# Kernel optimization log

Measured on AMD Instinct MI355X. Metric: run time of the kernel, lower is better.

The kernel has to match this reference:

```python
import jax, jax.numpy as jnp
import numpy as np

B, S, D = 8, 512, 256          # batch, seq_len, input_depth
E, H = 8, 4                    # num_experts, num_heads
DK = DV = DO = 256             # total_key/value/output depth (per expert)
DH = DK // H                   # head dim = 64
SCALE = DH ** -0.5


def setup_inputs() -> dict:
    key = jax.random.key(0)
    ks = jax.random.split(key, 8)
    queries = jax.random.normal(ks[0], (B, S, D), jnp.float32)
    keys = jax.random.normal(ks[1], (B, S, D), jnp.float32)
    values = jax.random.normal(ks[2], (B, S, D), jnp.float32)
    mask = jax.random.randint(ks[3], (B, S, S), 0, 2).astype(bool)
    s = 0.05
    Wq = jax.random.normal(ks[4], (D, DK * E), jnp.float32) * s
    Wk = jax.random.normal(ks[5], (D, DK * E), jnp.float32) * s
    Wv = jax.random.normal(ks[6], (D, DV * E), jnp.float32) * s
    Wo = jax.random.normal(ks[7], (DV, DO * E), jnp.float32) * s
    return {"queries": queries, "keys": keys, "values": values, "mask": mask,
            "Wq": Wq, "Wk": Wk, "Wv": Wv, "Wo": Wo}


def _split_heads(x):
    # [B, S, E*H*DH] -> [B, E, H, S, DH]
    b, s, _ = x.shape
    return x.reshape(b, s, E, H, -1).transpose(0, 2, 3, 1, 4)


def reference(queries, keys, values, mask, Wq, Wk, Wv, Wo):
    q = _split_heads(queries @ Wq) * SCALE   # [B,E,H,S,DH]
    k = _split_heads(keys @ Wk)
    v = _split_heads(values @ Wv)
    logits = jnp.einsum('behqd,behkd->behqk', q, k)      # [B,E,H,S,S]
    m = mask[:, None, None].astype(jnp.float32)          # [B,1,1,S,S]
    logits = logits * (1.0 - m) + (-1e18) * m
    w = jax.nn.softmax(logits, axis=-1)
    ctx = jnp.einsum('behqk,behkd->behqd', w, v)         # [B,E,H,S,DH]
    # merge heads -> [B, S, E, H*DH]
    ctx = ctx.transpose(0, 3, 1, 2, 4).reshape(B, S, E, H * DH)
    # faithful quirk: Dense applied on rank-4 tensor -> [B,S,E,DO*E]
    return ctx @ Wo
```

## Files before the change

kernel.cpp:

```cpp
#include <hip/hip_runtime.h>
#include <stdint.h>


typedef __bf16 bf16x8 __attribute__((ext_vector_type(8)));
typedef float f32x4 __attribute__((ext_vector_type(4)));
typedef unsigned short u16x8 __attribute__((ext_vector_type(8)));
typedef unsigned short u16x4 __attribute__((ext_vector_type(4)));

#define MFMA16(a, b, c) __builtin_amdgcn_mfma_f32_16x16x32_bf16(a, b, c, 0, 0, 0)

__device__ __forceinline__ unsigned short bfc(float x) {
    __bf16 b = (__bf16)x;
    return __builtin_bit_cast(unsigned short, b);
}

__device__ __forceinline__ void gload16(const void* g, void* l) {
    __builtin_amdgcn_global_load_lds(
        (const __attribute__((address_space(1))) void*)g,
        (__attribute__((address_space(3))) void*)l, 16, 0, 0);
}

#define QSCALE 0.18033688011112042f
#define MASKVAL -28.853900817779268f

__global__ __launch_bounds__(256) void prep_kern(
        const float* __restrict__ q, const float* __restrict__ k,
        const float* __restrict__ v, const int* __restrict__ mask,
        const float* __restrict__ Wq, const float* __restrict__ Wk,
        const float* __restrict__ Wv, const float* __restrict__ Wo,
        unsigned short* __restrict__ qb, unsigned short* __restrict__ kb,
        unsigned short* __restrict__ vb, unsigned short* __restrict__ wt,
        uint32_t* __restrict__ maskbits) {
    __shared__ float tile[32][33];
    const int x = blockIdx.x, t = threadIdx.x;
    if (x < 3072) {
        int which = x >> 10;
        const float* s = (which == 0) ? q : (which == 1) ? k : v;
        unsigned short* o = (which == 0) ? qb : (which == 1) ? kb : vb;
        int i = ((x & 1023) * 256 + t) * 4;
        float4 f = *(const float4*)&s[i];
        u16x4 r;
        r[0] = bfc(f.x); r[1] = bfc(f.y); r[2] = bfc(f.z); r[3] = bfc(f.w);
        *(u16x4*)&o[i] = r;
    } else if (x < 5120) {
        int y = x - 3072;
        int wsel = y >> 9;
        const float* W = (wsel == 0) ? Wq : (wsel == 1) ? Wk : (wsel == 2) ? Wv : Wo;
        unsigned short* T = wt + wsel * 2048 * 256;
        int rem = y & 511;
        int c0 = (rem & 63) * 32, r0 = (rem >> 6) * 32;
        int tr = t >> 3, tc = (t & 7) * 4;
        float4 f = *(const float4*)&W[(r0 + tr) * 2048 + c0 + tc];
        tile[tr][tc + 0] = f.x; tile[tr][tc + 1] = f.y;
        tile[tr][tc + 2] = f.z; tile[tr][tc + 3] = f.w;
        __syncthreads();
        u16x4 o;
        o[0] = bfc(tile[tc + 0][tr]); o[1] = bfc(tile[tc + 1][tr]);
        o[2] = bfc(tile[tc + 2][tr]); o[3] = bfc(tile[tc + 3][tr]);
        *(u16x4*)&T[(c0 + tr) * 256 + r0 + tc] = o;
    } else {
        const int lane = t & 63;
        int wi = ((x - 5120) * 4 + (t >> 6)) * 32;
        for (int i = 0; i < 32; ++i) {
            int u = wi + i;
            int b = u >> 12, rem = u & 4095, row = rem >> 3, ktp = rem & 7;
            int mv = mask[((size_t)(b * 512 + row)) * 512 + ktp * 64 + lane];
            unsigned long long bal = __ballot(mv != 0);
            if (lane == 0) {
                maskbits[(size_t)(b * 16 + ktp * 2) * 512 + row] = (uint32_t)bal;
                maskbits[(size_t)(b * 16 + ktp * 2 + 1) * 512 + row] = (uint32_t)(bal >> 32);
            }
        }
    }
}

__global__ __launch_bounds__(1024) void fused_kern(
        const unsigned short* __restrict__ actq,
        const unsigned short* __restrict__ actk,
        const unsigned short* __restrict__ actv,
        const unsigned short* __restrict__ Wt,
        const uint32_t* __restrict__ maskbits,
        unsigned short* __restrict__ CTX) {
    __shared__ unsigned short Klds[512 * 64];
    __shared__ unsigned short Vt[64 * 512];
    __shared__ unsigned short R3[2][64 * 128];
    const int bid = (int)blockIdx.x;
    const int flat = (bid & 7) * 32 + (bid >> 3);
    const int b = flat >> 5, eh = flat & 31;
    const int e = eh >> 2, h = eh & 3;
    const int t = threadIdx.x, w = t >> 6, l = t & 63, li = l & 15, g = l >> 4;
    const int tw0 = w * 32;
    const size_t actoff = (size_t)b * 512 * 256;
    const size_t wso = ((size_t)(e * 256 + h * 64)) * 256;

    bf16x8 qf[2][2];

    auto STAGEW = [&](int unit) {
        const unsigned short* W = Wt + (size_t)(unit >> 1) * 2048 * 256 + wso +
                                  (unit & 1) * 128;
        const int nr = (w << 2) + (l >> 4), cic = l & 15;
        gload16(&W[(size_t)nr * 256 + ((cic ^ (nr & 7)) << 3)],
                &R3[unit & 1][w * 512]);
    };

    STAGEW(0);
    __syncthreads();

    for (int p = 0; p < 3; ++p) {
        const unsigned short* A = ((p == 0) ? actq : (p == 1) ? actk : actv) + actoff;
        f32x4 acc[2][4];
#pragma unroll
        for (int m = 0; m < 2; ++m)
#pragma unroll
            for (int n = 0; n < 4; ++n) acc[m][n] = (f32x4){0.f, 0.f, 0.f, 0.f};
#pragma unroll
        for (int kh = 0; kh < 2; ++kh) {
            const int unit = p * 2 + kh;
            if (unit < 5) STAGEW(unit + 1);
            const unsigned short* cur = R3[unit & 1];
#pragma unroll
            for (int kk = 0; kk < 4; ++kk) {
                const int k0 = kh * 128 + kk * 32;
                bf16x8 af[2], bfr[4];
#pragma unroll
                for (int m = 0; m < 2; ++m)
                    af[m] = *(const bf16x8*)&A[(size_t)(tw0 + m * 16 + li) * 256 + k0 + g * 8];
#pragma unroll
                for (int n = 0; n < 4; ++n) {
                    int nr = n * 16 + li;
                    bfr[n] = *(const bf16x8*)&cur[nr * 128 + ((kk * 32 + g * 8) ^ ((nr & 7) << 3))];
                }
                if (p == 2) {
#pragma unroll
                    for (int m = 0; m < 2; ++m)
#pragma unroll
                        for (int n = 0; n < 4; ++n)
                            acc[m][n] = MFMA16(af[m], bfr[n], acc[m][n]);
                } else {
#pragma unroll
                    for (int m = 0; m < 2; ++m)
#pragma unroll
                        for (int n = 0; n < 4; ++n)
                            acc[m][n] = MFMA16(bfr[n], af[m], acc[m][n]);
                }
            }
            __syncthreads();
        }
        if (p == 0) {
            unsigned short* qs = Klds + w * 2048;
#pragma unroll
            for (int m = 0; m < 2; ++m)
#pragma unroll
                for (int n = 0; n < 4; ++n) {
                    int row = m * 16 + li, dh = n * 16 + g * 4;
                    u16x4 o;
#pragma unroll
                    for (int i = 0; i < 4; ++i) o[i] = bfc(acc[m][n][i] * QSCALE);
                    *(u16x4*)&qs[row * 64 + (dh ^ ((row & 7) << 3))] = o;
                }
#pragma unroll
            for (int m = 0; m < 2; ++m) {
                int row = m * 16 + li;
                qf[m][0] = *(const bf16x8*)&qs[row * 64 + ((g * 8) ^ ((row & 7) << 3))];
                qf[m][1] = *(const bf16x8*)&qs[row * 64 + ((32 + g * 8) ^ ((row & 7) << 3))];
            }
        } else if (p == 1) {
#pragma unroll
            for (int m = 0; m < 2; ++m)
#pragma unroll
                for (int n = 0; n < 4; ++n) {
                    int tok = tw0 + m * 16 + li, dh = n * 16 + g * 4;
                    u16x4 o;
#pragma unroll
                    for (int i = 0; i < 4; ++i) o[i] = bfc(acc[m][n][i]);
                    *(u16x4*)&Klds[tok * 64 + (dh ^ (((tok >> 1) & 7) << 3))] = o;
                }
        } else {
#pragma unroll
            for (int m = 0; m < 2; ++m)
#pragma unroll
                for (int n = 0; n < 4; ++n) {
                    int tok = tw0 + m * 16 + g * 4, dh = n * 16 + li;
                    u16x4 o;
#pragma unroll
                    for (int i = 0; i < 4; ++i) o[i] = bfc(acc[m][n][i]);
                    *(u16x4*)&Vt[dh * 512 + (tok ^ ((dh & 7) << 3))] = o;
                }
        }
    }
    __syncthreads();

    bf16x8 vaug;
#pragma unroll
    for (int j = 0; j < 8; ++j) vaug[j] = (li == 0) ? (__bf16)1.0f : (__bf16)0.0f;
    f32x4 atc[2][4], lacc[2];
#pragma unroll
    for (int m = 0; m < 2; ++m) {
#pragma unroll
        for (int c = 0; c < 4; ++c) atc[m][c] = (f32x4){0.f, 0.f, 0.f, 0.f};
        lacc[m] = (f32x4){0.f, 0.f, 0.f, 0.f};
    }
    unsigned short* Pw = &R3[0][0] + w * 512;
    const uint32_t* mb = maskbits + (size_t)b * 16 * 512;

    for (int kt = 0; kt < 16; ++kt) {
        bf16x8 kf[2][2];
#pragma unroll
        for (int f = 0; f < 2; ++f) {
            int tok = kt * 32 + 2 * li + f;
            const unsigned short* kr = &Klds[tok * 64];
            int sw = ((tok >> 1) & 7) << 3;
            kf[f][0] = *(const bf16x8*)&kr[(g * 8) ^ sw];
            kf[f][1] = *(const bf16x8*)&kr[(32 + g * 8) ^ sw];
        }
        f32x4 s[2][2];
#pragma unroll
        for (int m = 0; m < 2; ++m)
#pragma unroll
            for (int f = 0; f < 2; ++f) {
                f32x4 zz = (f32x4){0.f, 0.f, 0.f, 0.f};
                zz = MFMA16(qf[m][0], kf[f][0], zz);
                zz = MFMA16(qf[m][1], kf[f][1], zz);
                s[m][f] = zz;
            }
#pragma unroll
        for (int m = 0; m < 2; ++m) {
            const uint4 mw = *(const uint4*)&mb[(size_t)kt * 512 +
                                                tw0 + m * 16 + g * 4];
#pragma unroll
            for (int i = 0; i < 4; ++i) {
                uint32_t word = (i == 0) ? mw.x : (i == 1) ? mw.y : (i == 2) ? mw.z : mw.w;
                uint32_t pair = (word >> (2 * li)) & 3u;
                if (pair & 1u) s[m][0][i] = MASKVAL;
                if (pair & 2u) s[m][1][i] = MASKVAL;
            }
        }
        bf16x8 bv[4];
#pragma unroll
        for (int c = 0; c < 4; ++c) {
            int dh = c * 16 + li;
            bv[c] = *(const bf16x8*)&Vt[dh * 512 + ((kt * 32 + g * 8) ^ ((dh & 7) << 3))];
        }
#pragma unroll
        for (int m = 0; m < 2; ++m) {
#pragma unroll
            for (int i = 0; i < 4; ++i) {
                int row = g * 4 + i;
                uint32_t pk = (uint32_t)bfc(__builtin_exp2f(s[m][0][i])) |
                              ((uint32_t)bfc(__builtin_exp2f(s[m][1][i])) << 16);
                *(uint32_t*)&Pw[row * 32 + ((2 * li) ^ ((row & 3) << 3))] = pk;
            }
            bf16x8 pa = *(const bf16x8*)&Pw[li * 32 + ((g * 8) ^ ((li & 3) << 3))];
#pragma unroll
            for (int c = 0; c < 4; ++c)
                atc[m][c] = MFMA16(bv[c], pa, atc[m][c]);
            lacc[m] = MFMA16(vaug, pa, lacc[m]);
        }
    }
#pragma unroll
    for (int m = 0; m < 2; ++m) {
        float l_i = __shfl(lacc[m][0], l & 15, 64);
        float inv = 1.0f / l_i;
        const int qrow = tw0 + m * 16 + li;
#pragma unroll
        for (int c = 0; c < 4; ++c) {
            u16x4 o;
#pragma unroll
            for (int i = 0; i < 4; ++i) o[i] = bfc(atc[m][c][i] * inv);
            *(u16x4*)&CTX[(size_t)((b * 512 + qrow) * 8 + e) * 256 +
                          h * 64 + c * 16 + g * 4] = o;
        }
    }
}

__global__ __launch_bounds__(256) void gemm_kern(
        const unsigned short* __restrict__ A,
        const unsigned short* __restrict__ Bt,
        float* __restrict__ C, int cpx) {
    __shared__ __align__(16) unsigned char smem[32768];
    unsigned short* Asl = (unsigned short*)smem;
    unsigned short* Bsl = (unsigned short*)(smem + 16384);
    const int bid = (int)blockIdx.x;
    const int logical = (bid & 7) * cpx + (bid >> 3);
    const int bx = logical & 15;
    const int by = logical >> 4;
    const int t = threadIdx.x, l = t & 63, w = t >> 6;
    const int li = l & 15, g = l >> 4;
    const int wr = w >> 1, wc = w & 1;
    const int rowA = by * 128, colB = bx * 128;
    f32x4 acc[4][4];
#pragma unroll
    for (int m = 0; m < 4; ++m)
#pragma unroll
        for (int n = 0; n < 4; ++n) acc[m][n] = (f32x4){0.f, 0.f, 0.f, 0.f};

    for (int kk = 0; kk < 4; ++kk) {
#pragma unroll
        for (int j = 0; j < 4; ++j) {
            const int seg = j * 4 + w;
            const int chunk = seg * 64 + l;
            const int row = chunk >> 3, c8 = chunk & 7;
            const int src8 = (c8 ^ (row & 7)) * 8;
            gload16(&A[(size_t)(rowA + row) * 256 + kk * 64 + src8],
                    &Asl[seg * 512]);
            gload16(&Bt[(size_t)(colB + row) * 256 + kk * 64 + src8],
                    &Bsl[seg * 512]);
        }
        __syncthreads();
#pragma unroll
        for (int hh = 0; hh < 2; ++hh) {
            bf16x8 af[4], bfr[4];
#pragma unroll
            for (int m = 0; m < 4; ++m) {
                int row = wr * 64 + m * 16 + li;
                af[m] = *(const bf16x8*)&Asl[row * 64 + (((hh * 4 + g) ^ (row & 7)) * 8)];
            }
#pragma unroll
            for (int n = 0; n < 4; ++n) {
                int row = wc * 64 + n * 16 + li;
                bfr[n] = *(const bf16x8*)&Bsl[row * 64 + (((hh * 4 + g) ^ (row & 7)) * 8)];
            }
#pragma unroll
            for (int m = 0; m < 4; ++m)
#pragma unroll
                for (int n = 0; n < 4; ++n)
                    acc[m][n] = MFMA16(bfr[n], af[m], acc[m][n]);
        }
        __syncthreads();
    }
    float* osl = (float*)smem;
    const int wb = w * 1088;
#pragma unroll
    for (int m = 0; m < 4; ++m) {
#pragma unroll
        for (int n = 0; n < 4; ++n) {
            int c16 = (n * 4 + g) ^ (li & 3);
            *(f32x4*)&osl[wb + li * 68 + c16 * 4] = acc[m][n];
        }
#pragma unroll
        for (int r = 0; r < 4; ++r) {
            int chunk = r * 64 + l;
            int row = chunk >> 4, cic = chunk & 15;
            f32x4 v = *(const f32x4*)&osl[wb + row * 68 + (cic ^ (row & 3)) * 4];
            const int rr = rowA + wr * 64 + m * 16 + row;
            const int cc = colB + wc * 64 + cic * 4;
            __builtin_nontemporal_store(v, (f32x4*)&C[(size_t)rr * 2048 + cc]);
        }
    }
}

extern "C" void kernel_launch(void* const* d_in, const int* in_sizes, int n_in,
                              void* d_out, int out_size, void* d_ws, size_t ws_size,
                              hipStream_t stream) {
    (void)in_sizes; (void)n_in; (void)out_size; (void)ws_size;
    const float* queries = (const float*)d_in[0];
    const float* keys    = (const float*)d_in[1];
    const float* values  = (const float*)d_in[2];
    const int*   mask    = (const int*)d_in[3];
    const float* Wq = (const float*)d_in[4];
    const float* Wk = (const float*)d_in[5];
    const float* Wv = (const float*)d_in[6];
    const float* Wo = (const float*)d_in[7];

    unsigned short* CTX = (unsigned short*)d_ws;
    unsigned short* Qbf = CTX + (size_t)32768 * 256;
    unsigned short* Wt  = Qbf + (size_t)3 * 4096 * 256;
    uint32_t* maskbits  = (uint32_t*)(Wt + (size_t)4 * 2048 * 256);

    prep_kern<<<dim3(5376), 256, 0, stream>>>(queries, keys, values, mask,
                                              Wq, Wk, Wv, Wo,
                                              Qbf, Qbf + 4096 * 256, Qbf + 2 * 4096 * 256,
                                              Wt, maskbits);
    fused_kern<<<dim3(256), 1024, 0, stream>>>(Qbf, Qbf + 4096 * 256,
                                               Qbf + 2 * 4096 * 256,
                                               Wt, maskbits, CTX);
    gemm_kern<<<dim3(4096), 256, 0, stream>>>(CTX, Wt + (size_t)3 * 2048 * 256,
                                              (float*)d_out, 512);
}
```

Before: 139.4 us.

## Restructure output GEMM: load full-K B tile to LDS once, stream A from global

The output projection GEMM now uses 128x64 tiles, twice as many blocks. Each block stages the whole 64x256 slice of Wo into LDS with a single barrier. The A operand (CTX) is read directly from global memory into registers, so the per-k-step LDS staging of A and the repeated syncthreads go away. The cost is uncoalesced, non-shared A reads from global memory (each A row is reread by 32 column blocks) and more blocks to schedule.

```diff
diff --git a/kernel.cpp b/kernel.cpp
--- a/kernel.cpp
+++ b/kernel.cpp
@@ -277,73 +277,64 @@
         const unsigned short* __restrict__ A,
         const unsigned short* __restrict__ Bt,
         float* __restrict__ C, int cpx) {
-    __shared__ __align__(16) unsigned char smem[32768];
-    unsigned short* Asl = (unsigned short*)smem;
-    unsigned short* Bsl = (unsigned short*)(smem + 16384);
+    __shared__ unsigned short Bsl[64 * 256];
+    __shared__ __align__(16) float bounce[4 * 1088];
     const int bid = (int)blockIdx.x;
     const int logical = (bid & 7) * cpx + (bid >> 3);
-    const int bx = logical & 15;
-    const int by = logical >> 4;
+    const int bx = logical & 31;
+    const int by = logical >> 5;
     const int t = threadIdx.x, l = t & 63, w = t >> 6;
     const int li = l & 15, g = l >> 4;
-    const int wr = w >> 1, wc = w & 1;
-    const int rowA = by * 128, colB = bx * 128;
-    f32x4 acc[4][4];
-#pragma unroll
-    for (int m = 0; m < 4; ++m)
+    const int rowA = by * 128, colB = bx * 64;
+
+#pragma unroll
+    for (int j = 0; j < 8; ++j) {
+        const int seg = j * 4 + w;
+        const int chunk = seg * 64 + l;
+        const int row = chunk >> 5, cic = chunk & 31;
+        gload16(&Bt[(size_t)(colB + row) * 256 + ((cic ^ (row & 7)) << 3)],
+                &Bsl[seg * 512]);
+    }
+    __syncthreads();
+
+    f32x4 acc[2][4];
+#pragma unroll
+    for (int m = 0; m < 2; ++m)
 #pragma unroll
         for (int n = 0; n < 4; ++n) acc[m][n] = (f32x4){0.f, 0.f, 0.f, 0.f};
 
-    for (int kk = 0; kk < 4; ++kk) {
-#pragma unroll
-        for (int j = 0; j < 4; ++j) {
-            const int seg = j * 4 + w;
-            const int chunk = seg * 64 + l;
-            const int row = chunk >> 3, c8 = chunk & 7;
-            const int src8 = (c8 ^ (row & 7)) * 8;
-            gload16(&A[(size_t)(rowA + row) * 256 + kk * 64 + src8],
-                    &Asl[seg * 512]);
-            gload16(&Bt[(size_t)(colB + row) * 256 + kk * 64 + src8],
-                    &Bsl[seg * 512]);
-        }
-        __syncthreads();
-#pragma unroll
-        for (int hh = 0; hh < 2; ++hh) {
-            bf16x8 af[4], bfr[4];
-#pragma unroll
-            for (int m = 0; m < 4; ++m) {
-                int row = wr * 64 + m * 16 + li;
-                af[m] = *(const bf16x8*)&Asl[row * 64 + (((hh * 4 + g) ^ (row & 7)) * 8)];
-            }
+#pragma unroll
+    for (int m = 0; m < 2; ++m) {
+        const int r = rowA + w * 32 + m * 16 + li;
+        bf16x8 af[8];
+#pragma unroll
+        for (int kk = 0; kk < 8; ++kk)
+            af[kk] = *(const bf16x8*)&A[(size_t)r * 256 + kk * 32 + g * 8];
+#pragma unroll
+        for (int kk = 0; kk < 8; ++kk)
 #pragma unroll
             for (int n = 0; n < 4; ++n) {
-                int row = wc * 64 + n * 16 + li;
-                bfr[n] = *(const bf16x8*)&Bsl[row * 64 + (((hh * 4 + g) ^ (row & 7)) * 8)];
-            }
-#pragma unroll
-            for (int m = 0; m < 4; ++m)
-#pragma unroll
-                for (int n = 0; n < 4; ++n)
-                    acc[m][n] = MFMA16(bfr[n], af[m], acc[m][n]);
-        }
-        __syncthreads();
-    }
-    float* osl = (float*)smem;
-    const int wb = w * 1088;
-#pragma unroll
-    for (int m = 0; m < 4; ++m) {
+                const int c = n * 16 + li;
+                bf16x8 b = *(const bf16x8*)&Bsl[c * 256 +
+                    (((kk * 4 + g) ^ (c & 7)) << 3)];
+                acc[m][n] = MFMA16(b, af[kk], acc[m][n]);
+            }
+    }
+    float* osl = bounce + w * 1088;
+#pragma unroll
+    for (int m = 0; m < 2; ++m) {
 #pragma unroll
         for (int n = 0; n < 4; ++n) {
             int c16 = (n * 4 + g) ^ (li & 3);
-            *(f32x4*)&osl[wb + li * 68 + c16 * 4] = acc[m][n];
-        }
-#pragma unroll
-        for (int r = 0; r < 4; ++r) {
-            int chunk = r * 64 + l;
+            *(f32x4*)&osl[li * 68 + c16 * 4] = acc[m][n];
+        }
+#pragma unroll
+        for (int r4 = 0; r4 < 4; ++r4) {
+            int chunk = r4 * 64 + l;
             int row = chunk >> 4, cic = chunk & 15;
-            f32x4 v = *(const f32x4*)&osl[wb + row * 68 + (cic ^ (row & 3)) * 4];
-            const int rr = rowA + wr * 64 + m * 16 + row;
-            const int cc = colB + wc * 64 + cic * 4;
+            f32x4 v = *(const f32x4*)&osl[row * 68 + ((cic ^ (row & 3)) * 4)];
+            const int rr = rowA + w * 32 + m * 16 + row;
+            const int cc = colB + cic * 4;
             __builtin_nontemporal_store(v, (f32x4*)&C[(size_t)rr * 2048 + cc]);
         }
     }
@@ -374,6 +365,6 @@
     fused_kern<<<dim3(256), 1024, 0, stream>>>(Qbf, Qbf + 4096 * 256,
                                                Qbf + 2 * 4096 * 256,
                                                Wt, maskbits, CTX);
-    gemm_kern<<<dim3(4096), 256, 0, stream>>>(CTX, Wt + (size_t)3 * 2048 * 256,
-                                              (float*)d_out, 512);
-}
+    gemm_kern<<<dim3(8192), 256, 0, stream>>>(CTX, Wt + (size_t)3 * 2048 * 256,
+                                              (float*)d_out, 1024);
+}
```

Result: slower. 171.5 us (median of 2 runs) (+23.1%).

## Halve fused attention block to 8 waves, each handling 64 query rows

Applied to the files above, without the earlier changes.

Cuts the fused attention kernel from 16 to 8 wavefronts per block and has each wave process 64 query rows instead of 32. K/V fragments and weight fragments loaded from LDS are then reused across twice as many MFMAs. Mask words are software-prefetched one key tile ahead, and the P-tile staging is reorganized so all four row blocks are written before reading. The cost is higher register pressure (doubled accumulators) and less latency hiding from fewer waves per CU.

```diff
diff --git a/kernel.cpp b/kernel.cpp
--- a/kernel.cpp
+++ b/kernel.cpp
@@ -74,7 +74,7 @@
     }
 }
 
-__global__ __launch_bounds__(1024) void fused_kern(
+__global__ __launch_bounds__(512) void fused_kern(
         const unsigned short* __restrict__ actq,
         const unsigned short* __restrict__ actk,
         const unsigned short* __restrict__ actv,
@@ -89,18 +89,22 @@
     const int b = flat >> 5, eh = flat & 31;
     const int e = eh >> 2, h = eh & 3;
     const int t = threadIdx.x, w = t >> 6, l = t & 63, li = l & 15, g = l >> 4;
-    const int tw0 = w * 32;
+    const int tw0 = w * 64;
     const size_t actoff = (size_t)b * 512 * 256;
     const size_t wso = ((size_t)(e * 256 + h * 64)) * 256;
 
-    bf16x8 qf[2][2];
+    bf16x8 qf[4][2];
 
     auto STAGEW = [&](int unit) {
         const unsigned short* W = Wt + (size_t)(unit >> 1) * 2048 * 256 + wso +
                                   (unit & 1) * 128;
-        const int nr = (w << 2) + (l >> 4), cic = l & 15;
-        gload16(&W[(size_t)nr * 256 + ((cic ^ (nr & 7)) << 3)],
-                &R3[unit & 1][w * 512]);
+#pragma unroll
+        for (int j = 0; j < 2; ++j) {
+            const int c = j * 512 + t;
+            const int nr = c >> 4, cic = c & 15;
+            gload16(&W[(size_t)nr * 256 + ((cic ^ (nr & 7)) << 3)],
+                    &R3[unit & 1][j * 4096 + w * 512]);
+        }
     };
 
     STAGEW(0);
@@ -108,9 +112,9 @@
 
     for (int p = 0; p < 3; ++p) {
         const unsigned short* A = ((p == 0) ? actq : (p == 1) ? actk : actv) + actoff;
-        f32x4 acc[2][4];
-#pragma unroll
-        for (int m = 0; m < 2; ++m)
+        f32x4 acc[4][4];
+#pragma unroll
+        for (int m = 0; m < 4; ++m)
 #pragma unroll
             for (int n = 0; n < 4; ++n) acc[m][n] = (f32x4){0.f, 0.f, 0.f, 0.f};
 #pragma unroll
@@ -121,9 +125,9 @@
 #pragma unroll
             for (int kk = 0; kk < 4; ++kk) {
                 const int k0 = kh * 128 + kk * 32;
-                bf16x8 af[2], bfr[4];
-#pragma unroll
-                for (int m = 0; m < 2; ++m)
+                bf16x8 af[4], bfr[4];
+#pragma unroll
+                for (int m = 0; m < 4; ++m)
                     af[m] = *(const bf16x8*)&A[(size_t)(tw0 + m * 16 + li) * 256 + k0 + g * 8];
 #pragma unroll
                 for (int n = 0; n < 4; ++n) {
@@ -132,13 +136,13 @@
                 }
                 if (p == 2) {
 #pragma unroll
-                    for (int m = 0; m < 2; ++m)
+                    for (int m = 0; m < 4; ++m)
 #pragma unroll
                         for (int n = 0; n < 4; ++n)
                             acc[m][n] = MFMA16(af[m], bfr[n], acc[m][n]);
                 } else {
 #pragma unroll
-                    for (int m = 0; m < 2; ++m)
+                    for (int m = 0; m < 4; ++m)
 #pragma unroll
                         for (int n = 0; n < 4; ++n)
                             acc[m][n] = MFMA16(bfr[n], af[m], acc[m][n]);
@@ -147,9 +151,9 @@
             __syncthreads();
         }
         if (p == 0) {
-            unsigned short* qs = Klds + w * 2048;
-#pragma unroll
-            for (int m = 0; m < 2; ++m)
+            unsigned short* qs = Klds + w * 4096;
+#pragma unroll
+            for (int m = 0; m < 4; ++m)
 #pragma unroll
                 for (int n = 0; n < 4; ++n) {
                     int row = m * 16 + li, dh = n * 16 + g * 4;
@@ -159,14 +163,14 @@
                     *(u16x4*)&qs[row * 64 + (dh ^ ((row & 7) << 3))] = o;
                 }
 #pragma unroll
-            for (int m = 0; m < 2; ++m) {
+            for (int m = 0; m < 4; ++m) {
                 int row = m * 16 + li;
                 qf[m][0] = *(const bf16x8*)&qs[row * 64 + ((g * 8) ^ ((row & 7) << 3))];
                 qf[m][1] = *(const bf16x8*)&qs[row * 64 + ((32 + g * 8) ^ ((row & 7) << 3))];
             }
         } else if (p == 1) {
 #pragma unroll
-            for (int m = 0; m < 2; ++m)
+            for (int m = 0; m < 4; ++m)
 #pragma unroll
                 for (int n = 0; n < 4; ++n) {
                     int tok = tw0 + m * 16 + li, dh = n * 16 + g * 4;
@@ -177,7 +181,7 @@
                 }
         } else {
 #pragma unroll
-            for (int m = 0; m < 2; ++m)
+            for (int m = 0; m < 4; ++m)
 #pragma unroll
                 for (int n = 0; n < 4; ++n) {
                     int tok = tw0 + m * 16 + g * 4, dh = n * 16 + li;
@@ -193,15 +197,20 @@
     bf16x8 vaug;
 #pragma unroll
     for (int j = 0; j < 8; ++j) vaug[j] = (li == 0) ? (__bf16)1.0f : (__bf16)0.0f;
-    f32x4 atc[2][4], lacc[2];
-#pragma unroll
-    for (int m = 0; m < 2; ++m) {
+    f32x4 atc[4][4], lacc[4];
+#pragma unroll
+    for (int m = 0; m < 4; ++m) {
 #pragma unroll
         for (int c = 0; c < 4; ++c) atc[m][c] = (f32x4){0.f, 0.f, 0.f, 0.f};
         lacc[m] = (f32x4){0.f, 0.f, 0.f, 0.f};
     }
-    unsigned short* Pw = &R3[0][0] + w * 512;
+    unsigned short* Pw = &R3[0][0] + w * 2048;
     const uint32_t* mb = maskbits + (size_t)b * 16 * 512;
+
+    uint4 mwn[4];
+#pragma unroll
+    for (int m = 0; m < 4; ++m)
+        mwn[m] = *(const uint4*)&mb[tw0 + m * 16 + g * 4];
 
     for (int kt = 0; kt < 16; ++kt) {
         bf16x8 kf[2][2];
@@ -209,13 +218,13 @@
         for (int f = 0; f < 2; ++f) {
             int tok = kt * 32 + 2 * li + f;
             const unsigned short* kr = &Klds[tok * 64];
-            int sw = ((tok >> 1) & 7) << 3;
+            int sw = (li & 7) << 3;
             kf[f][0] = *(const bf16x8*)&kr[(g * 8) ^ sw];
             kf[f][1] = *(const bf16x8*)&kr[(32 + g * 8) ^ sw];
         }
-        f32x4 s[2][2];
-#pragma unroll
-        for (int m = 0; m < 2; ++m)
+        f32x4 s[4][2];
+#pragma unroll
+        for (int m = 0; m < 4; ++m)
 #pragma unroll
             for (int f = 0; f < 2; ++f) {
                 f32x4 zz = (f32x4){0.f, 0.f, 0.f, 0.f};
@@ -224,17 +233,29 @@
                 s[m][f] = zz;
             }
 #pragma unroll
-        for (int m = 0; m < 2; ++m) {
-            const uint4 mw = *(const uint4*)&mb[(size_t)kt * 512 +
-                                                tw0 + m * 16 + g * 4];
+        for (int m = 0; m < 4; ++m)
 #pragma unroll
             for (int i = 0; i < 4; ++i) {
-                uint32_t word = (i == 0) ? mw.x : (i == 1) ? mw.y : (i == 2) ? mw.z : mw.w;
+                uint32_t word = (i == 0) ? mwn[m].x : (i == 1) ? mwn[m].y
+                              : (i == 2) ? mwn[m].z : mwn[m].w;
                 uint32_t pair = (word >> (2 * li)) & 3u;
                 if (pair & 1u) s[m][0][i] = MASKVAL;
                 if (pair & 2u) s[m][1][i] = MASKVAL;
             }
-        }
+        if (kt < 15) {
+#pragma unroll
+            for (int m = 0; m < 4; ++m)
+                mwn[m] = *(const uint4*)&mb[(size_t)(kt + 1) * 512 + tw0 + m * 16 + g * 4];
+        }
+#pragma unroll
+        for (int m = 0; m < 4; ++m)
+#pragma unroll
+            for (int i = 0; i < 4; ++i) {
+                int row = m * 16 + g * 4 + i;
+                uint32_t pk = (uint32_t)bfc(__builtin_exp2f(s[m][0][i])) |
+                              ((uint32_t)bfc(__builtin_exp2f(s[m][1][i])) << 16);
+                *(uint32_t*)&Pw[row * 32 + ((((li >> 2) ^ (row & 3)) << 3) + 2 * (li & 3))] = pk;
+            }
         bf16x8 bv[4];
 #pragma unroll
         for (int c = 0; c < 4; ++c) {
@@ -242,15 +263,9 @@
             bv[c] = *(const bf16x8*)&Vt[dh * 512 + ((kt * 32 + g * 8) ^ ((dh & 7) << 3))];
         }
 #pragma unroll
-        for (int m = 0; m < 2; ++m) {
-#pragma unroll
-            for (int i = 0; i < 4; ++i) {
-                int row = g * 4 + i;
-                uint32_t pk = (uint32_t)bfc(__builtin_exp2f(s[m][0][i])) |
-                              ((uint32_t)bfc(__builtin_exp2f(s[m][1][i])) << 16);
-                *(uint32_t*)&Pw[row * 32 + ((2 * li) ^ ((row & 3) << 3))] = pk;
-            }
-            bf16x8 pa = *(const bf16x8*)&Pw[li * 32 + ((g * 8) ^ ((li & 3) << 3))];
+        for (int m = 0; m < 4; ++m) {
+            int rm = m * 16 + li;
+            bf16x8 pa = *(const bf16x8*)&Pw[rm * 32 + ((g ^ (rm & 3)) << 3)];
 #pragma unroll
             for (int c = 0; c < 4; ++c)
                 atc[m][c] = MFMA16(bv[c], pa, atc[m][c]);
@@ -258,7 +273,7 @@
         }
     }
 #pragma unroll
-    for (int m = 0; m < 2; ++m) {
+    for (int m = 0; m < 4; ++m) {
         float l_i = __shfl(lacc[m][0], l & 15, 64);
         float inv = 1.0f / l_i;
         const int qrow = tw0 + m * 16 + li;
@@ -371,9 +386,9 @@
                                               Wq, Wk, Wv, Wo,
                                               Qbf, Qbf + 4096 * 256, Qbf + 2 * 4096 * 256,
                                               Wt, maskbits);
-    fused_kern<<<dim3(256), 1024, 0, stream>>>(Qbf, Qbf + 4096 * 256,
-                                               Qbf + 2 * 4096 * 256,
-                                               Wt, maskbits, CTX);
+    fused_kern<<<dim3(256), 512, 0, stream>>>(Qbf, Qbf + 4096 * 256,
+                                              Qbf + 2 * 4096 * 256,
+                                              Wt, maskbits, CTX);
     gemm_kern<<<dim3(4096), 256, 0, stream>>>(CTX, Wt + (size_t)3 * 2048 * 256,
                                               (float*)d_out, 512);
 }
```

After: 141.4 us. Within noise of the previous version (+1.5%).
